# Performance work log

Hardware: AMD Instinct MI355X
Metric: run time of the kernel (lower is better)

Reference implementation:

```python
import jax, jax.numpy as jnp
import numpy as np

H = 64   # hidden_dim
E = 5    # num_edge_features
F = 6    # num_node_features
B, W, N = 8, 12, 200
LN_EPS = 1e-5


def _lstm_layer(x, Wih, Whh, bih, bhh):
    # x: [BN, W, Fin] -> full output sequence [BN, W, H] (PyTorch gate order i,f,g,o)
    BN = x.shape[0]
    h0 = jnp.zeros((BN, Whh.shape[1]), x.dtype)
    def step(carry, xt):
        h, c = carry
        g = xt @ Wih.T + h @ Whh.T + (bih + bhh)
        i, f, gg, o = jnp.split(g, 4, axis=-1)
        c = jax.nn.sigmoid(f) * c + jax.nn.sigmoid(i) * jnp.tanh(gg)
        h = jax.nn.sigmoid(o) * jnp.tanh(c)
        return (h, c), h
    _, ys = jax.lax.scan(step, (h0, h0), jnp.swapaxes(x, 0, 1))
    return jnp.swapaxes(ys, 0, 1)


def _layernorm(x, g, b):
    mu = jnp.mean(x, axis=-1, keepdims=True)
    var = jnp.mean(jnp.square(x - mu), axis=-1, keepdims=True)
    return (x - mu) * jax.lax.rsqrt(var + LN_EPS) * g + b


def setup_inputs() -> dict:
    key = jax.random.key(0)
    ks = jax.random.split(key, 32)
    s = 0.05
    d = {
        'node_features': jax.random.normal(ks[0], (B, W, N, F), jnp.float32),
        'edge_features': jax.random.normal(ks[1], (B, W, N, N, E), jnp.float32),
        'adjacency': jax.random.uniform(ks[2], (B, N, N), jnp.float32),
        # LSTM layer 0 (input F) and layer 1 (input H)
        'Wih0': jax.random.normal(ks[3], (4 * H, F), jnp.float32) * s,
        'Whh0': jax.random.normal(ks[4], (4 * H, H), jnp.float32) * s,
        'bih0': jax.random.normal(ks[5], (4 * H,), jnp.float32) * s,
        'bhh0': jax.random.normal(ks[6], (4 * H,), jnp.float32) * s,
        'Wih1': jax.random.normal(ks[7], (4 * H, H), jnp.float32) * s,
        'Whh1': jax.random.normal(ks[8], (4 * H, H), jnp.float32) * s,
        'bih1': jax.random.normal(ks[9], (4 * H,), jnp.float32) * s,
        'bhh1': jax.random.normal(ks[10], (4 * H,), jnp.float32) * s,
        # 2 GCN layers: linear, edge projection, layernorm
        'gcn_W': jax.random.normal(ks[11], (2, H, H), jnp.float32) * s,
        'gcn_b': jax.random.normal(ks[12], (2, H), jnp.float32) * s,
        'ep_W': jax.random.normal(ks[13], (2, H, E), jnp.float32) * s,
        'ep_b': jax.random.normal(ks[14], (2, H), jnp.float32) * s,
        'ln_g': jnp.ones((2, H), jnp.float32),
        'ln_b': jnp.zeros((2, H), jnp.float32),
        # edge MLP: (2H+E) -> H -> H//2 -> 1
        'mlp_W1': jax.random.normal(ks[15], (H, 2 * H + E), jnp.float32) * s,
        'mlp_b1': jax.random.normal(ks[16], (H,), jnp.float32) * s,
        'mlp_W2': jax.random.normal(ks[17], (H // 2, H), jnp.float32) * s,
        'mlp_b2': jax.random.normal(ks[18], (H // 2,), jnp.float32) * s,
        'mlp_W3': jax.random.normal(ks[19], (1, H // 2), jnp.float32) * s,
        'mlp_b3': jax.random.normal(ks[20], (1,), jnp.float32) * s,
    }
    return d


def reference(node_features, edge_features, adjacency,
              Wih0, Whh0, bih0, bhh0, Wih1, Whh1, bih1, bhh1,
              gcn_W, gcn_b, ep_W, ep_b, ln_g, ln_b,
              mlp_W1, mlp_b1, mlp_W2, mlp_b2, mlp_W3, mlp_b3):
    Bn, Wn, Nn, _ = node_features.shape
    # [B,W,N,F] -> [B*N, W, F]
    x = jnp.transpose(node_features, (0, 2, 1, 3)).reshape(Bn * Nn, Wn, -1)
    y0 = _lstm_layer(x, Wih0, Whh0, bih0, bhh0)      # dropout between layers: eval mode (identity)
    y1 = _lstm_layer(y0, Wih1, Whh1, bih1, bhh1)
    h = y1[:, -1, :].reshape(Bn, Nn, H)

    edge_last = edge_features[:, -1]                 # [B,N,N,E]
    for i in range(2):
        edge_h = edge_last @ ep_W[i].T + ep_b[i]     # [B,N,N,H]
        messages = jnp.einsum('bij,bijn->bin', adjacency, edge_h)
        updated = h @ gcn_W[i].T + gcn_b[i] + messages
        h = jax.nn.relu(_layernorm(updated, ln_g[i], ln_b[i]))
        # dropout: eval mode (identity)

    h_i = jnp.broadcast_to(h[:, :, None, :], (Bn, Nn, Nn, H))
    h_j = jnp.broadcast_to(h[:, None, :, :], (Bn, Nn, Nn, H))
    edge_input = jnp.concatenate([h_i, h_j, edge_last], axis=-1)  # [B,N,N,2H+E]
    z = jax.nn.relu(edge_input @ mlp_W1.T + mlp_b1)
    z = jax.nn.relu(z @ mlp_W2.T + mlp_b2)
    logits = (z @ mlp_W3.T + mlp_b3)[..., 0]
    return jax.nn.sigmoid(logits)
```

## Files before the change

kernel.cpp:

```cpp
#include <hip/hip_runtime.h>
#include <math.h>


#define Hd   64
#define Ed   5
#define Fd   6
#define Bd   8
#define Wd   12
#define Nd   200
#define NSEQ (Bd*Nd)
#define NG   (4*Hd)
#define NEDGE (Bd*Nd*Nd)
#define LNEPS 1e-5f

#define PIN4(v) asm volatile("" : "+v"((v).x), "+v"((v).y), "+v"((v).z), "+v"((v).w))

__device__ __forceinline__ float sigm(float x) { return 1.0f / (1.0f + __expf(-x)); }
__device__ __forceinline__ float tanh_fast(float x) {
  float ax = fabsf(x);
  float t  = __expf(-2.0f * ax);
  float r  = (1.0f - t) / (1.0f + t);
  return copysignf(r, x);
}

__global__ __launch_bounds__(256) void k_prep(const float* __restrict__ Wih1,
                                              float* __restrict__ Wt1) {
  int k = blockIdx.x;
  int j = threadIdx.x;
  Wt1[k * NG + j] = Wih1[j * Hd + k];
}

__global__ __launch_bounds__(256, 3) void k_lstm0(
    const float* __restrict__ nf,
    const float* __restrict__ Wih0, const float* __restrict__ Whh0,
    const float* __restrict__ bih0, const float* __restrict__ bhh0,
    float* __restrict__ y0)
{
  __shared__ float x_sh[Wd * Fd];
  __shared__ float h_sh[Hd];
  __shared__ float gate_sh[2][NG];

  const int tid = threadIdx.x;
  const int seq = blockIdx.x;
  const int b = seq / Nd, n = seq % Nd;
  const int u = tid & 63;

  if (tid < Wd * Fd) {
    int t = tid / Fd, f = tid % Fd;
    x_sh[tid] = nf[((b * Wd + t) * Nd + n) * Fd + f];
  }
  h_sh[u] = 0.f;

  const int j = tid;
  float4 wh[16];
  const float4* wrow = (const float4*)(Whh0 + j * Hd);
  #pragma unroll
  for (int q = 0; q < 16; ++q) { wh[q] = wrow[q]; PIN4(wh[q]); }
  float wx[Fd];
  #pragma unroll
  for (int f = 0; f < Fd; ++f) wx[f] = Wih0[j * Fd + f];
  const float bias = bih0[j] + bhh0[j];
  const int jt = j >> 6;

  float c = 0.f;
  __syncthreads();

  for (int t = 0; t < Wd; ++t) {
    const float* xp = x_sh + t * Fd;
    float a0 = bias, a1 = 0.f, a2 = 0.f, a3 = 0.f;
    #pragma unroll
    for (int f = 0; f < Fd; ++f) a1 += xp[f] * wx[f];
    const float4* h4 = (const float4*)h_sh;
    #pragma unroll
    for (int q = 0; q < 16; ++q) {
      float4 hv = h4[q];
      float d = hv.x * wh[q].x + hv.y * wh[q].y + hv.z * wh[q].z + hv.w * wh[q].w;
      if ((q & 3) == 0) a0 += d; else if ((q & 3) == 1) a1 += d;
      else if ((q & 3) == 2) a2 += d; else a3 += d;
    }
    float acc = (a0 + a1) + (a2 + a3);
    gate_sh[t & 1][j] = (jt == 2) ? tanh_fast(acc) : sigm(acc);
    __syncthreads();
    const float* gb = gate_sh[t & 1];
    float iv = gb[u];
    float fv = gb[64 + u];
    float gv = gb[128 + u];
    float ov = gb[192 + u];
    c = fv * c + iv * gv;
    float h = ov * tanh_fast(c);
    h_sh[u] = h;
    if (tid < Hd) y0[seq * (Wd * Hd) + t * Hd + u] = h;
  }
}

__global__ __launch_bounds__(256) void k_xproj1(
    const float* __restrict__ y0,
    const float* __restrict__ Wt1,
    const float* __restrict__ bih1, const float* __restrict__ bhh1,
    float* __restrict__ G1)
{
  __shared__ float ysh[64 * 65];
  __shared__ float osh[2 * 64 * 65];

  const int tid  = threadIdx.x;
  const int row0 = blockIdx.x * 64;
  for (int idx = tid; idx < 64 * 64; idx += 256) {
    int r = idx >> 6, k = idx & 63;
    ysh[r * 65 + k] = y0[(row0 + r) * Hd + k];
  }
  __syncthreads();

  const int w = __builtin_amdgcn_readfirstlane(tid >> 6);
  const int r = tid & 63;
  float acc[64];
  #pragma unroll
  for (int c = 0; c < 64; ++c) acc[c] = 0.f;

  const float* wbase = Wt1 + (w << 6);
  #pragma unroll 2
  for (int k = 0; k < 64; ++k) {
    float yv = ysh[r * 65 + k];
    const float* wk = wbase + k * NG;
    #pragma unroll
    for (int c = 0; c < 64; ++c) acc[c] = fmaf(yv, wk[c], acc[c]);
  }
  #pragma unroll
  for (int c = 0; c < 64; ++c) acc[c] += bih1[(w << 6) + c] + bhh1[(w << 6) + c];

  #pragma unroll
  for (int p = 0; p < 2; ++p) {
    __syncthreads();
    if ((w >> 1) == p) {
      float* orow = osh + ((w & 1) * 64 + r) * 65;
      #pragma unroll
      for (int c = 0; c < 64; ++c) orow[c] = acc[c];
    }
    __syncthreads();
    for (int idx = tid; idx < 2 * 64 * 64; idx += 256) {
      int c  = idx & 127;
      int rr = idx >> 7;
      G1[(row0 + rr) * NG + p * 128 + c] =
          osh[((c >> 6) * 64 + rr) * 65 + (c & 63)];
    }
  }
}

__global__ __launch_bounds__(256, 3) void k_lstm1(
    const float* __restrict__ G1,
    const float* __restrict__ Whh1,
    float* __restrict__ hout)
{
  __shared__ float h_sh[Hd];
  __shared__ float gate_sh[2][NG];

  const int tid = threadIdx.x;
  const int seq = blockIdx.x;
  const int u = tid & 63;
  h_sh[u] = 0.f;

  const int j = tid;
  float4 wh[16];
  const float4* wrow = (const float4*)(Whh1 + j * Hd);
  #pragma unroll
  for (int q = 0; q < 16; ++q) { wh[q] = wrow[q]; PIN4(wh[q]); }
  const int jt = j >> 6;
  float c = 0.f;

  float g_cur = G1[(seq * Wd + 0) * NG + j];
  __syncthreads();

  for (int t = 0; t < Wd; ++t) {
    float g_next = (t + 1 < Wd) ? G1[(seq * Wd + t + 1) * NG + j] : 0.f;
    float a0 = g_cur;
    float a1 = 0.f, a2 = 0.f, a3 = 0.f;
    const float4* h4 = (const float4*)h_sh;
    #pragma unroll
    for (int q = 0; q < 16; ++q) {
      float4 hv = h4[q];
      float d = hv.x * wh[q].x + hv.y * wh[q].y + hv.z * wh[q].z + hv.w * wh[q].w;
      if ((q & 3) == 0) a0 += d; else if ((q & 3) == 1) a1 += d;
      else if ((q & 3) == 2) a2 += d; else a3 += d;
    }
    float acc = (a0 + a1) + (a2 + a3);
    gate_sh[t & 1][j] = (jt == 2) ? tanh_fast(acc) : sigm(acc);
    __syncthreads();
    const float* gb = gate_sh[t & 1];
    float iv = gb[u];
    float fv = gb[64 + u];
    float gv = gb[128 + u];
    float ov = gb[192 + u];
    c = fv * c + iv * gv;
    float h = ov * tanh_fast(c);
    h_sh[u] = h;
    if (t == Wd - 1 && tid < Hd) hout[seq * Hd + u] = h;
    g_cur = g_next;
  }
}

__global__ __launch_bounds__(256) void k_node(
    const float* __restrict__ ef,    const float* __restrict__ adj,
    const float* __restrict__ h0,
    const float* __restrict__ gcn_W, const float* __restrict__ gcn_b,
    const float* __restrict__ ep_W,  const float* __restrict__ ep_b,
    const float* __restrict__ ln_g,  const float* __restrict__ ln_b,
    const float* __restrict__ W1,    const float* __restrict__ b1,
    float* __restrict__ uu, float* __restrict__ vt)
{
  __shared__ float red[4][6];
  __shared__ float w6[6];
  __shared__ float hcur[Hd];

  const int row = blockIdx.x;
  const int b = row / Nd, i = row % Nd;
  const int tid = threadIdx.x;

  float p[6] = {0.f, 0.f, 0.f, 0.f, 0.f, 0.f};
  if (tid < Nd) {
    float a = adj[(b * Nd + i) * Nd + tid];
    const float* e = ef + (((b * Wd + (Wd - 1)) * Nd + i) * Nd + tid) * Ed;
    p[5] = a;
    #pragma unroll
    for (int k = 0; k < Ed; ++k) p[k] = a * e[k];
  }
  #pragma unroll
  for (int k = 0; k < 6; ++k) {
    float v = p[k];
    for (int off = 32; off > 0; off >>= 1) v += __shfl_down(v, off);
    p[k] = v;
  }
  if ((tid & 63) == 0) {
    #pragma unroll
    for (int k = 0; k < 6; ++k) red[tid >> 6][k] = p[k];
  }
  __syncthreads();
  if (tid < 6)
    w6[tid] = red[0][tid] + red[1][tid] + red[2][tid] + red[3][tid];
  if (tid < Hd) hcur[tid] = h0[row * Hd + tid];
  __syncthreads();

  const int u = tid & 63;
  #pragma unroll
  for (int round = 0; round < 2; ++round) {
    float hnew = 0.f;
    if (tid < 64) {
      const float* gw = gcn_W + (round * Hd + u) * Hd;
      const float* ew = ep_W  + (round * Hd + u) * Ed;
      float acc = gcn_b[round * Hd + u] + w6[5] * ep_b[round * Hd + u];
      #pragma unroll
      for (int e = 0; e < Ed; ++e) acc += w6[e] * ew[e];
      #pragma unroll 8
      for (int k = 0; k < Hd; ++k) acc += hcur[k] * gw[k];

      float mu = acc;
      #pragma unroll
      for (int off = 1; off < 64; off <<= 1) mu += __shfl_xor(mu, off);
      mu *= (1.f / 64.f);
      float d = acc - mu;
      float var = d * d;
      #pragma unroll
      for (int off = 1; off < 64; off <<= 1) var += __shfl_xor(var, off);
      var *= (1.f / 64.f);
      float v = d * rsqrtf(var + LNEPS) * ln_g[round * Hd + u] + ln_b[round * Hd + u];
      hnew = fmaxf(v, 0.f);
    }
    __syncthreads();
    if (tid < 64) hcur[tid] = hnew;
    __syncthreads();
  }

  if (tid < 64) {
    const float* wr = W1 + tid * 133;
    float acc = b1[tid];
    #pragma unroll 8
    for (int k = 0; k < Hd; ++k) acc += hcur[k] * wr[k];
    uu[row * Hd + tid] = acc;
  } else if (tid < 128) {
    const int n = tid - 64;
    const float* wr = W1 + n * 133 + 64;
    float acc = 0.f;
    #pragma unroll 8
    for (int k = 0; k < Hd; ++k) acc += hcur[k] * wr[k];
    vt[n * NSEQ + row] = acc;
  }
}

__global__ __launch_bounds__(256) void k_mlp(
    const float* __restrict__ ef,
    const float* __restrict__ u, const float* __restrict__ vt,
    const float* __restrict__ W1,
    const float* __restrict__ W2, const float* __restrict__ b2,
    const float* __restrict__ W3, const float* __restrict__ b3,
    float* __restrict__ out)
{
  const int idx = blockIdx.x * 256 + threadIdx.x;
  const int b   = idx / (Nd * Nd);
  const int rem = idx - b * Nd * Nd;
  const int i   = rem / Nd;
  const int jj  = rem - i * Nd;

  const float* e = ef + (((b * Wd + (Wd - 1)) * Nd + i) * Nd + jj) * Ed;
  float e5[Ed];
  #pragma unroll
  for (int q = 0; q < Ed; ++q) e5[q] = e[q];

  const float* ur = u + (b * Nd + i) * Hd;
  const int vcol = b * Nd + jj;

  float z1[64];
  #pragma unroll
  for (int k = 0; k < 64; ++k) {
    float acc = ur[k] + vt[k * NSEQ + vcol];
    const float* w1c = W1 + k * 133 + 128;
    #pragma unroll
    for (int q = 0; q < Ed; ++q) acc += e5[q] * w1c[q];
    z1[k] = fmaxf(acc, 0.f);
  }

  float logit = b3[0];
  #pragma unroll 4
  for (int o = 0; o < 32; ++o) {
    float a0 = b2[o], a1 = 0.f, a2 = 0.f, a3 = 0.f;
    const float* w2 = W2 + o * 64;
    #pragma unroll
    for (int k = 0; k < 64; k += 4) {
      a0 += w2[k]     * z1[k];
      a1 += w2[k + 1] * z1[k + 1];
      a2 += w2[k + 2] * z1[k + 2];
      a3 += w2[k + 3] * z1[k + 3];
    }
    float z2 = fmaxf((a0 + a1) + (a2 + a3), 0.f);
    logit += W3[o] * z2;
  }
  out[idx] = 1.f / (1.f + __expf(-logit));
}

extern "C" void kernel_launch(void* const* d_in, const int* in_sizes, int n_in,
                              void* d_out, int out_size, void* d_ws, size_t ws_size,
                              hipStream_t stream) {
  (void)in_sizes; (void)n_in; (void)out_size; (void)ws_size;
  const float* nf   = (const float*)d_in[0];
  const float* ef   = (const float*)d_in[1];
  const float* adj  = (const float*)d_in[2];
  const float* Wih0 = (const float*)d_in[3];
  const float* Whh0 = (const float*)d_in[4];
  const float* bih0 = (const float*)d_in[5];
  const float* bhh0 = (const float*)d_in[6];
  const float* Wih1 = (const float*)d_in[7];
  const float* Whh1 = (const float*)d_in[8];
  const float* bih1 = (const float*)d_in[9];
  const float* bhh1 = (const float*)d_in[10];
  const float* gcnW = (const float*)d_in[11];
  const float* gcnB = (const float*)d_in[12];
  const float* epW  = (const float*)d_in[13];
  const float* epB  = (const float*)d_in[14];
  const float* lnG  = (const float*)d_in[15];
  const float* lnB  = (const float*)d_in[16];
  const float* W1   = (const float*)d_in[17];
  const float* b1   = (const float*)d_in[18];
  const float* W2   = (const float*)d_in[19];
  const float* b2   = (const float*)d_in[20];
  const float* W3   = (const float*)d_in[21];
  const float* b3   = (const float*)d_in[22];
  float* out = (float*)d_out;

  float* ws  = (float*)d_ws;
  float* y0  = ws;
  float* G1  = y0  + 1228800;
  float* Wt1 = G1  + 4915200;
  float* h0  = Wt1 + 16384;
  float* uu  = h0  + 102400;
  float* vt  = uu  + 102400;

  k_prep  <<<64,   256, 0, stream>>>(Wih1, Wt1);
  k_lstm0 <<<NSEQ, 256, 0, stream>>>(nf, Wih0, Whh0, bih0, bhh0, y0);
  k_xproj1<<<300,  256, 0, stream>>>(y0, Wt1, bih1, bhh1, G1);
  k_lstm1 <<<NSEQ, 256, 0, stream>>>(G1, Whh1, h0);
  k_node  <<<1600, 256, 0, stream>>>(ef, adj, h0, gcnW, gcnB, epW, epB,
                                     lnG, lnB, W1, b1, uu, vt);
  k_mlp   <<<1250, 256, 0, stream>>>(ef, uu, vt, W1, W2, b2, W3, b3, out);
}
```

Before: 282.5 us.

## Batch four LSTM sequences per block to reuse register-held recurrent weights

Both LSTM kernels now process four sequences per block instead of one, so each thread's 64 recurrent weights loaded into registers are reused across four sequences. This cuts the number of weight loads by a factor of four and shrinks the grid. In exchange, the serial per-step work per block grows fourfold, an extra barrier is added each step, and occupancy hints drop from 3 to 2. The weight loads now go through volatile pointers instead of asm pinning, and the grid drops to 400 blocks, which may leave compute units underused.

```diff
diff --git a/kernel.cpp b/kernel.cpp
--- a/kernel.cpp
+++ b/kernel.cpp
@@ -11,9 +11,8 @@
 #define NSEQ (Bd*Nd)
 #define NG   (4*Hd)
 #define NEDGE (Bd*Nd*Nd)
+#define SEQB 4
 #define LNEPS 1e-5f
-
-#define PIN4(v) asm volatile("" : "+v"((v).x), "+v"((v).y), "+v"((v).z), "+v"((v).w))
 
 __device__ __forceinline__ float sigm(float x) { return 1.0f / (1.0f + __expf(-x)); }
 __device__ __forceinline__ float tanh_fast(float x) {
@@ -30,66 +29,79 @@
   Wt1[k * NG + j] = Wih1[j * Hd + k];
 }
 
-__global__ __launch_bounds__(256, 3) void k_lstm0(
+__global__ __launch_bounds__(256, 2) void k_lstm0(
     const float* __restrict__ nf,
     const float* __restrict__ Wih0, const float* __restrict__ Whh0,
     const float* __restrict__ bih0, const float* __restrict__ bhh0,
     float* __restrict__ y0)
 {
-  __shared__ float x_sh[Wd * Fd];
-  __shared__ float h_sh[Hd];
-  __shared__ float gate_sh[2][NG];
-
-  const int tid = threadIdx.x;
-  const int seq = blockIdx.x;
-  const int b = seq / Nd, n = seq % Nd;
-  const int u = tid & 63;
-
-  if (tid < Wd * Fd) {
-    int t = tid / Fd, f = tid % Fd;
-    x_sh[tid] = nf[((b * Wd + t) * Nd + n) * Fd + f];
-  }
-  h_sh[u] = 0.f;
+  __shared__ float x_sh[SEQB * Wd * Fd];
+  __shared__ float h_sh[SEQB][Hd];
+  __shared__ float gate_sh[SEQB][NG];
+
+  const int tid  = threadIdx.x;
+  const int seq0 = blockIdx.x * SEQB;
+
+  for (int idx = tid; idx < SEQB * Wd * Fd; idx += 256) {
+    int s = idx / (Wd * Fd); int rem = idx % (Wd * Fd);
+    int t = rem / Fd;        int f   = rem % Fd;
+    int seq = seq0 + s; int b = seq / Nd; int n = seq % Nd;
+    x_sh[idx] = nf[((b * Wd + t) * Nd + n) * Fd + f];
+  }
+  if (tid < SEQB * Hd) h_sh[tid >> 6][tid & 63] = 0.f;
 
   const int j = tid;
-  float4 wh[16];
-  const float4* wrow = (const float4*)(Whh0 + j * Hd);
-  #pragma unroll
-  for (int q = 0; q < 16; ++q) { wh[q] = wrow[q]; PIN4(wh[q]); }
+  float wreg[Hd];
+  {
+    const volatile float* wp = Whh0 + j * Hd;
+    #pragma unroll
+    for (int k = 0; k < Hd; ++k) wreg[k] = wp[k];
+  }
   float wx[Fd];
-  #pragma unroll
-  for (int f = 0; f < Fd; ++f) wx[f] = Wih0[j * Fd + f];
+  {
+    const volatile float* xp = Wih0 + j * Fd;
+    #pragma unroll
+    for (int f = 0; f < Fd; ++f) wx[f] = xp[f];
+  }
   const float bias = bih0[j] + bhh0[j];
   const int jt = j >> 6;
 
+  const int su = tid >> 6;
+  const int uu = tid & 63;
   float c = 0.f;
   __syncthreads();
 
   for (int t = 0; t < Wd; ++t) {
-    const float* xp = x_sh + t * Fd;
-    float a0 = bias, a1 = 0.f, a2 = 0.f, a3 = 0.f;
-    #pragma unroll
-    for (int f = 0; f < Fd; ++f) a1 += xp[f] * wx[f];
-    const float4* h4 = (const float4*)h_sh;
-    #pragma unroll
-    for (int q = 0; q < 16; ++q) {
-      float4 hv = h4[q];
-      float d = hv.x * wh[q].x + hv.y * wh[q].y + hv.z * wh[q].z + hv.w * wh[q].w;
-      if ((q & 3) == 0) a0 += d; else if ((q & 3) == 1) a1 += d;
-      else if ((q & 3) == 2) a2 += d; else a3 += d;
-    }
-    float acc = (a0 + a1) + (a2 + a3);
-    gate_sh[t & 1][j] = (jt == 2) ? tanh_fast(acc) : sigm(acc);
-    __syncthreads();
-    const float* gb = gate_sh[t & 1];
-    float iv = gb[u];
-    float fv = gb[64 + u];
-    float gv = gb[128 + u];
-    float ov = gb[192 + u];
-    c = fv * c + iv * gv;
-    float h = ov * tanh_fast(c);
-    h_sh[u] = h;
-    if (tid < Hd) y0[seq * (Wd * Hd) + t * Hd + u] = h;
+    #pragma unroll
+    for (int s = 0; s < SEQB; ++s) {
+      const float* xp = x_sh + (s * Wd + t) * Fd;
+      float a0 = bias, a1 = 0.f, a2 = 0.f, a3 = 0.f;
+      #pragma unroll
+      for (int f = 0; f < Fd; ++f) a1 += xp[f] * wx[f];
+      const float4* h4 = (const float4*)h_sh[s];
+      #pragma unroll
+      for (int q = 0; q < 16; ++q) {
+        float4 hv = h4[q];
+        float d = hv.x * wreg[4 * q]     + hv.y * wreg[4 * q + 1] +
+                  hv.z * wreg[4 * q + 2] + hv.w * wreg[4 * q + 3];
+        if ((q & 3) == 0) a0 += d; else if ((q & 3) == 1) a1 += d;
+        else if ((q & 3) == 2) a2 += d; else a3 += d;
+      }
+      float acc = (a0 + a1) + (a2 + a3);
+      gate_sh[s][j] = (jt == 2) ? tanh_fast(acc) : sigm(acc);
+    }
+    __syncthreads();
+    {
+      float iv = gate_sh[su][uu];
+      float fv = gate_sh[su][64 + uu];
+      float gv = gate_sh[su][128 + uu];
+      float ov = gate_sh[su][192 + uu];
+      c = fv * c + iv * gv;
+      float h = ov * tanh_fast(c);
+      h_sh[su][uu] = h;
+      y0[(seq0 + su) * (Wd * Hd) + t * Hd + uu] = h;
+    }
+    __syncthreads();
   }
 }
 
@@ -145,55 +157,72 @@
   }
 }
 
-__global__ __launch_bounds__(256, 3) void k_lstm1(
+__global__ __launch_bounds__(256, 2) void k_lstm1(
     const float* __restrict__ G1,
     const float* __restrict__ Whh1,
     float* __restrict__ hout)
 {
-  __shared__ float h_sh[Hd];
-  __shared__ float gate_sh[2][NG];
-
-  const int tid = threadIdx.x;
-  const int seq = blockIdx.x;
-  const int u = tid & 63;
-  h_sh[u] = 0.f;
+  __shared__ float h_sh[SEQB][Hd];
+  __shared__ float gate_sh[SEQB][NG];
+
+  const int tid  = threadIdx.x;
+  const int seq0 = blockIdx.x * SEQB;
+  if (tid < SEQB * Hd) h_sh[tid >> 6][tid & 63] = 0.f;
 
   const int j = tid;
-  float4 wh[16];
-  const float4* wrow = (const float4*)(Whh1 + j * Hd);
-  #pragma unroll
-  for (int q = 0; q < 16; ++q) { wh[q] = wrow[q]; PIN4(wh[q]); }
+  float wreg[Hd];
+  {
+    const volatile float* wp = Whh1 + j * Hd;
+    #pragma unroll
+    for (int k = 0; k < Hd; ++k) wreg[k] = wp[k];
+  }
   const int jt = j >> 6;
+  const int su = tid >> 6;
+  const int uu = tid & 63;
   float c = 0.f;
 
-  float g_cur = G1[(seq * Wd + 0) * NG + j];
+  float gc[SEQB];
+  #pragma unroll
+  for (int s = 0; s < SEQB; ++s)
+    gc[s] = G1[((seq0 + s) * Wd + 0) * NG + j];
   __syncthreads();
 
   for (int t = 0; t < Wd; ++t) {
-    float g_next = (t + 1 < Wd) ? G1[(seq * Wd + t + 1) * NG + j] : 0.f;
-    float a0 = g_cur;
-    float a1 = 0.f, a2 = 0.f, a3 = 0.f;
-    const float4* h4 = (const float4*)h_sh;
-    #pragma unroll
-    for (int q = 0; q < 16; ++q) {
-      float4 hv = h4[q];
-      float d = hv.x * wh[q].x + hv.y * wh[q].y + hv.z * wh[q].z + hv.w * wh[q].w;
-      if ((q & 3) == 0) a0 += d; else if ((q & 3) == 1) a1 += d;
-      else if ((q & 3) == 2) a2 += d; else a3 += d;
-    }
-    float acc = (a0 + a1) + (a2 + a3);
-    gate_sh[t & 1][j] = (jt == 2) ? tanh_fast(acc) : sigm(acc);
-    __syncthreads();
-    const float* gb = gate_sh[t & 1];
-    float iv = gb[u];
-    float fv = gb[64 + u];
-    float gv = gb[128 + u];
-    float ov = gb[192 + u];
-    c = fv * c + iv * gv;
-    float h = ov * tanh_fast(c);
-    h_sh[u] = h;
-    if (t == Wd - 1 && tid < Hd) hout[seq * Hd + u] = h;
-    g_cur = g_next;
+    float gn[SEQB];
+    #pragma unroll
+    for (int s = 0; s < SEQB; ++s)
+      gn[s] = (t + 1 < Wd) ? G1[((seq0 + s) * Wd + t + 1) * NG + j] : 0.f;
+
+    #pragma unroll
+    for (int s = 0; s < SEQB; ++s) {
+      float a0 = gc[s];
+      float a1 = 0.f, a2 = 0.f, a3 = 0.f;
+      const float4* h4 = (const float4*)h_sh[s];
+      #pragma unroll
+      for (int q = 0; q < 16; ++q) {
+        float4 hv = h4[q];
+        float d = hv.x * wreg[4 * q]     + hv.y * wreg[4 * q + 1] +
+                  hv.z * wreg[4 * q + 2] + hv.w * wreg[4 * q + 3];
+        if ((q & 3) == 0) a0 += d; else if ((q & 3) == 1) a1 += d;
+        else if ((q & 3) == 2) a2 += d; else a3 += d;
+      }
+      float acc = (a0 + a1) + (a2 + a3);
+      gate_sh[s][j] = (jt == 2) ? tanh_fast(acc) : sigm(acc);
+    }
+    __syncthreads();
+    {
+      float iv = gate_sh[su][uu];
+      float fv = gate_sh[su][64 + uu];
+      float gv = gate_sh[su][128 + uu];
+      float ov = gate_sh[su][192 + uu];
+      c = fv * c + iv * gv;
+      float h = ov * tanh_fast(c);
+      h_sh[su][uu] = h;
+      if (t == Wd - 1) hout[(seq0 + su) * Hd + uu] = h;
+    }
+    __syncthreads();
+    #pragma unroll
+    for (int s = 0; s < SEQB; ++s) gc[s] = gn[s];
   }
 }
 
@@ -371,11 +400,11 @@
   float* uu  = h0  + 102400;
   float* vt  = uu  + 102400;
 
-  k_prep  <<<64,   256, 0, stream>>>(Wih1, Wt1);
-  k_lstm0 <<<NSEQ, 256, 0, stream>>>(nf, Wih0, Whh0, bih0, bhh0, y0);
-  k_xproj1<<<300,  256, 0, stream>>>(y0, Wt1, bih1, bhh1, G1);
-  k_lstm1 <<<NSEQ, 256, 0, stream>>>(G1, Whh1, h0);
-  k_node  <<<1600, 256, 0, stream>>>(ef, adj, h0, gcnW, gcnB, epW, epB,
-                                     lnG, lnB, W1, b1, uu, vt);
-  k_mlp   <<<1250, 256, 0, stream>>>(ef, uu, vt, W1, W2, b2, W3, b3, out);
-}
+  k_prep  <<<64,        256, 0, stream>>>(Wih1, Wt1);
+  k_lstm0 <<<NSEQ/SEQB, 256, 0, stream>>>(nf, Wih0, Whh0, bih0, bhh0, y0);
+  k_xproj1<<<300,       256, 0, stream>>>(y0, Wt1, bih1, bhh1, G1);
+  k_lstm1 <<<NSEQ/SEQB, 256, 0, stream>>>(G1, Whh1, h0);
+  k_node  <<<1600,      256, 0, stream>>>(ef, adj, h0, gcnW, gcnB, epW, epB,
+                                          lnG, lnB, W1, b1, uu, vt);
+  k_mlp   <<<1250,      256, 0, stream>>>(ef, uu, vt, W1, W2, b2, W3, b3, out);
+}
```

Measured after the change: 318.6 us. 12.8% more time.
